# Kernel optimization log

Hardware: AMD Instinct MI355X
Metric: run time of the kernel (lower is better)

## Reference

```python
import jax, jax.numpy as jnp
import numpy as np

B, S, D_H, D_L, K, K_H, W = 4, 4096, 1024, 256, 64, 4, 9


def setup_inputs() -> dict:
    key = jax.random.key(0)
    ks = jax.random.split(key, 6)
    return {
        "inputs": jax.random.normal(ks[0], (B, S, D_H), jnp.float32),
        "W1": jax.random.normal(ks[1], (D_H, D_L), jnp.float32) * 0.02,
        "b1": jnp.zeros((D_L,), jnp.float32),
        "RME": jax.random.normal(ks[2], (D_L, K), jnp.float32),
        "K2": jax.random.normal(ks[3], (K_H, D_L, D_L), jnp.float32) * 0.02,
        "b2": jnp.zeros((D_L,), jnp.float32),
        "Wu": jax.random.normal(ks[4], (D_L, D_H), jnp.float32) * 0.02,
        "bu": jnp.zeros((D_H,), jnp.float32),
        "gamma": jnp.ones((D_H,), jnp.float32),
        "beta": jnp.zeros((D_H,), jnp.float32),
    }


def _memory_reorg(act, RMVs, k_h):
    # act: [B,S,d_l], RMVs: [B,S,k]
    R = jnp.transpose(RMVs, (0, 2, 1))  # [B,k,S]
    h_vars = jnp.mean((R - jnp.mean(R, axis=-1, keepdims=True)) ** 2, axis=-1)  # [B,k]
    top = jnp.argsort(-h_vars, axis=-1)[:, :k_h]                   # [B,k_h]
    h_max = jnp.take_along_axis(R, top[:, :, None], axis=1)        # [B,k_h,S]
    perm = jnp.argsort(h_max, axis=-1)                             # [B,k_h,S] permutation indices
    g = jnp.take_along_axis(act[:, None], perm[..., None], axis=2) # [B,k_h,S,d_l]
    return jnp.transpose(g, (0, 2, 1, 3))                          # [B,S,k_h,d_l]


def reference(inputs, W1, b1, RME, K2, b2, Wu, bu, gamma, beta):
    # DOWN_PROJECTION_1
    q = jax.nn.relu(jnp.einsum('bsh,hd->bsd', inputs, W1) + b1)    # [B,S,d_l]
    # RANDOM_PROJECTION
    RMVs = jnp.einsum('bsd,dk->bsk', q, RME)                       # [B,S,k]
    # Memory reorganization (variance-based argsort permutations)
    qp = _memory_reorg(q, RMVs, K_H)                               # [B,S,k_h,d_l]
    # DOWN_PROJECTION_2
    q2 = jax.nn.relu(jnp.einsum('bskd,kde->bse', qp, K2) + b2)     # [B,S,d_l]
    # Sliding-window key construction (edge windows replicated)
    half = (W - 1) // 2
    widx = jnp.arange(S - W + 1)[:, None] + jnp.arange(W)[None, :]  # [S-W+1, W]
    win = q2[:, widx]                                               # [B,S-W+1,W,d_l]
    first = jnp.broadcast_to(q2[:, None, :W], (B, half, W, D_L))
    last = jnp.broadcast_to(q2[:, None, S - W:], (B, half, W, D_L))
    keyt = jnp.concatenate([first, win, last], axis=1)              # [B,S,W,d_l]
    # Windowed attention
    f = jnp.sqrt(jnp.float32(D_L))
    scores = jax.nn.softmax(jnp.einsum('bsd,bswd->bsw', q2, keyt) / f, axis=-1)  # [B,S,W]
    # UP_PROJECTION on keys -> values
    val = jax.nn.relu(jnp.einsum('bswd,dh->bswh', keyt, Wu) + bu)   # [B,S,W,d_h]
    out = jnp.einsum('bswh,bsw->bsh', val, scores)                  # [B,S,d_h]
    # LayerNorm (keras default epsilon=1e-3) on residual
    x = out + inputs
    mu = jnp.mean(x, axis=-1, keepdims=True)
    var = jnp.mean((x - mu) ** 2, axis=-1, keepdims=True)
    return gamma * (x - mu) * jax.lax.rsqrt(var + 1e-3) + beta
```

## Files before the change

### kernel.cpp

```cpp
#include <hip/hip_runtime.h>

#define B_  4
#define S_  4096
#define DH  1024
#define DL  256
#define KK  64
#define KH  4
#define WW  9

typedef unsigned short ushort_t;
typedef _Float16 f16;
typedef _Float16 f16x8 __attribute__((ext_vector_type(8)));
typedef float  f32x4  __attribute__((ext_vector_type(4)));

__device__ __forceinline__ void gld_lds16(const void* g, void* lds_uniform_base) {
    __builtin_amdgcn_global_load_lds(
        (const __attribute__((address_space(1))) unsigned int*)g,
        (__attribute__((address_space(3))) unsigned int*)lds_uniform_base,
        16, 0, 0);
}

__global__ __launch_bounds__(256)
void mfma_gemm2(const float* __restrict__ Af,
                const ushort_t* __restrict__ Bh, const ushort_t* __restrict__ Bl,
                const float* __restrict__ bias, float* __restrict__ C,
                ushort_t* __restrict__ Ch, int K, int N, int nbx)
{
    __shared__ __align__(16) ushort_t Abuf[64 * 64 * 2];
    __shared__ __align__(16) ushort_t Bsh[128 * 64];
    __shared__ __align__(16) ushort_t Bsl[128 * 64];

    const int tid = threadIdx.x;
    const int w = tid >> 6, l = tid & 63;
    const int wm = w >> 1, wn = w & 1;
    const int lr = l & 15, lk = l >> 4;
    const int cpx = gridDim.x >> 3;
    const int orig = (blockIdx.x & 7) * cpx + (blockIdx.x >> 3);
    const int m0 = (orig / nbx) * 64, n0 = (orig % nbx) * 128;

    f32x4 acc0[2][4] = {};
    f32x4 acc1[2][4] = {};

    for (int k0 = 0; k0 < K; k0 += 64) {
        {
            float* Asf = (float*)Abuf;
            #pragma unroll
            for (int it = 0; it < 4; ++it) {
                const int c = it * 256 + tid;
                const int r = c >> 4, cc = c & 15;
                const int hsw = ((r & 7) << 1) | ((r >> 3) & 1);
                const int cs = cc ^ hsw;
                const float* src = Af + (size_t)(m0 + r) * K + k0 + cs * 4;
                gld_lds16(src, &Asf[(size_t)c * 4]);
            }
        }
        #pragma unroll
        for (int it = 0; it < 4; ++it) {
            const int c = it * 256 + tid;
            const int r = c >> 3, kp = c & 7;
            const int kl = kp ^ (r & 7);
            const size_t off = (size_t)(n0 + r) * K + k0 + kl * 8;
            gld_lds16(Bh + off, &Bsh[(size_t)c * 8]);
            gld_lds16(Bl + off, &Bsl[(size_t)c * 8]);
        }
        __syncthreads();

        #pragma unroll
        for (int ks = 0; ks < 2; ++ks) {
            f16x8 ah[2], al[2];
            #pragma unroll
            for (int mf = 0; mf < 2; ++mf) {
                const int row = wm * 32 + mf * 16 + lr;
                const int kb  = ks * 4 + lk;
                const float* Asf = (const float*)Abuf;
                const int base = row * 64 + ((kb ^ (row & 7)) << 3);
                const int sw = ((row >> 3) & 1) << 2;
                const f32x4 lo = *(const f32x4*)&Asf[base + sw];
                const f32x4 hi = *(const f32x4*)&Asf[base + (4 - sw)];
                const float xs[8] = {lo[0], lo[1], lo[2], lo[3],
                                     hi[0], hi[1], hi[2], hi[3]};
                #pragma unroll
                for (int e = 0; e < 8; ++e) {
                    const f16 h = (f16)xs[e];
                    const f16 lv = (f16)((xs[e] - (float)h) * 2048.0f);
                    ah[mf][e] = h;
                    al[mf][e] = lv;
                }
            }
            #pragma unroll
            for (int nf = 0; nf < 4; ++nf) {
                const int row = wn * 64 + nf * 16 + lr;
                const int kb  = ks * 4 + lk;
                const int o   = row * 64 + ((kb ^ (row & 7)) << 3);
                const f16x8 bh = *(const f16x8*)&Bsh[o];
                const f16x8 bl = *(const f16x8*)&Bsl[o];
                #pragma unroll
                for (int mf = 0; mf < 2; ++mf) {
                    acc0[mf][nf] = __builtin_amdgcn_mfma_f32_16x16x32_f16(
                        ah[mf], bh, acc0[mf][nf], 0, 0, 0);
                    acc1[mf][nf] = __builtin_amdgcn_mfma_f32_16x16x32_f16(
                        ah[mf], bl, acc1[mf][nf], 0, 0, 0);
                    acc1[mf][nf] = __builtin_amdgcn_mfma_f32_16x16x32_f16(
                        al[mf], bh, acc1[mf][nf], 0, 0, 0);
                }
            }
        }
        __syncthreads();
    }

    float bv[4];
    #pragma unroll
    for (int nf = 0; nf < 4; ++nf)
        bv[nf] = bias[n0 + wn * 64 + nf * 16 + lr];
    #pragma unroll
    for (int mf = 0; mf < 2; ++mf)
        #pragma unroll
        for (int nf = 0; nf < 4; ++nf)
            #pragma unroll
            for (int r = 0; r < 4; ++r) {
                const int m = m0 + wm * 32 + mf * 16 + lk * 4 + r;
                const int n = n0 + wn * 64 + nf * 16 + lr;
                float x = acc0[mf][nf][r] + acc1[mf][nf][r] * (1.0f / 2048.0f) + bv[nf];
                x = fmaxf(x, 0.f);
                C[(size_t)m * N + n] = x;
                const f16 h = (f16)x;
                Ch[(size_t)m * N + n] = __builtin_bit_cast(ushort_t, h);
            }
}

__global__ __launch_bounds__(256)
void gemm6_1l(const ushort_t* __restrict__ Ah, const ushort_t* __restrict__ Bh,
              const float* __restrict__ bias, ushort_t* __restrict__ Ch,
              const int* __restrict__ gidx, int K, int N, int nbx)
{
    __shared__ __align__(16) ushort_t Ash[64 * 64];
    __shared__ __align__(16) ushort_t Bsh[128 * 64];

    const int tid = threadIdx.x;
    const int w = tid >> 6, l = tid & 63;
    const int wm = w >> 1, wn = w & 1;
    const int lr = l & 15, lk = l >> 4;
    const int cpx = gridDim.x >> 3;
    const int orig = (blockIdx.x & 7) * cpx + (blockIdx.x >> 3);
    const int m0 = (orig / nbx) * 64, n0 = (orig % nbx) * 128;

    f32x4 acc0[2][4] = {};

    for (int k0 = 0; k0 < K; k0 += 64) {
        #pragma unroll
        for (int it = 0; it < 2; ++it) {
            const int c = it * 256 + tid;
            const int r = c >> 3, kp = c & 7;
            const int kl = kp ^ (r & 7);
            const int rg = gidx[(m0 + r) * KH + (k0 >> 8)];
            const size_t off = (size_t)rg * DL + (k0 & (DL - 1)) + kl * 8;
            gld_lds16(Ah + off, &Ash[(size_t)c * 8]);
        }
        #pragma unroll
        for (int it = 0; it < 4; ++it) {
            const int c = it * 256 + tid;
            const int r = c >> 3, kp = c & 7;
            const int kl = kp ^ (r & 7);
            const size_t off = (size_t)(n0 + r) * K + k0 + kl * 8;
            gld_lds16(Bh + off, &Bsh[(size_t)c * 8]);
        }
        __syncthreads();

        #pragma unroll
        for (int ks = 0; ks < 2; ++ks) {
            f16x8 ah[2];
            #pragma unroll
            for (int mf = 0; mf < 2; ++mf) {
                const int row = wm * 32 + mf * 16 + lr;
                const int kb  = ks * 4 + lk;
                ah[mf] = *(const f16x8*)&Ash[row * 64 + ((kb ^ (row & 7)) << 3)];
            }
            #pragma unroll
            for (int nf = 0; nf < 4; ++nf) {
                const int row = wn * 64 + nf * 16 + lr;
                const int kb  = ks * 4 + lk;
                const f16x8 bh = *(const f16x8*)&Bsh[row * 64 + ((kb ^ (row & 7)) << 3)];
                #pragma unroll
                for (int mf = 0; mf < 2; ++mf)
                    acc0[mf][nf] = __builtin_amdgcn_mfma_f32_16x16x32_f16(
                        ah[mf], bh, acc0[mf][nf], 0, 0, 0);
            }
        }
        __syncthreads();
    }

    float bv[4];
    #pragma unroll
    for (int nf = 0; nf < 4; ++nf)
        bv[nf] = bias[n0 + wn * 64 + nf * 16 + lr];
    #pragma unroll
    for (int mf = 0; mf < 2; ++mf)
        #pragma unroll
        for (int nf = 0; nf < 4; ++nf)
            #pragma unroll
            for (int r = 0; r < 4; ++r) {
                const int m = m0 + wm * 32 + mf * 16 + lk * 4 + r;
                const int n = n0 + wn * 64 + nf * 16 + lr;
                float x = acc0[mf][nf][r] + bv[nf];
                x = fmaxf(x, 0.f);
                const f16 h = (f16)x;
                Ch[(size_t)m * N + n] = __builtin_bit_cast(ushort_t, h);
            }
}

__global__ __launch_bounds__(512)
void mfma_gemm1l(const ushort_t* __restrict__ Ah, const ushort_t* __restrict__ Bh,
                 const float* __restrict__ bias, ushort_t* __restrict__ Ch,
                 int K, int N, int nbx)
{
    __shared__ __align__(16) ushort_t Ash[128 * 64];
    __shared__ __align__(16) ushort_t Bsh[128 * 64];

    const int tid = threadIdx.x;
    const int w = tid >> 6, l = tid & 63;
    const int wm = w >> 1, wn = w & 1;
    const int lr = l & 15, lk = l >> 4;
    const int cpx = gridDim.x >> 3;
    const int orig = (blockIdx.x & 7) * cpx + (blockIdx.x >> 3);
    const int m0 = (orig / nbx) * 128, n0 = (orig % nbx) * 128;

    f32x4 acc0[2][4] = {};

    for (int k0 = 0; k0 < K; k0 += 64) {
        #pragma unroll
        for (int it = 0; it < 2; ++it) {
            const int c = it * 512 + tid;
            const int r = c >> 3, kp = c & 7;
            const int kl = kp ^ (r & 7);
            const size_t offA = (size_t)(m0 + r) * K + k0 + kl * 8;
            const size_t offB = (size_t)(n0 + r) * K + k0 + kl * 8;
            gld_lds16(Ah + offA, &Ash[(size_t)c * 8]);
            gld_lds16(Bh + offB, &Bsh[(size_t)c * 8]);
        }
        __syncthreads();

        #pragma unroll
        for (int ks = 0; ks < 2; ++ks) {
            f16x8 ah[2];
            #pragma unroll
            for (int mf = 0; mf < 2; ++mf) {
                const int row = wm * 32 + mf * 16 + lr;
                const int kb  = ks * 4 + lk;
                ah[mf] = *(const f16x8*)&Ash[row * 64 + ((kb ^ (row & 7)) << 3)];
            }
            #pragma unroll
            for (int nf = 0; nf < 4; ++nf) {
                const int row = wn * 64 + nf * 16 + lr;
                const int kb  = ks * 4 + lk;
                const f16x8 bh = *(const f16x8*)&Bsh[row * 64 + ((kb ^ (row & 7)) << 3)];
                #pragma unroll
                for (int mf = 0; mf < 2; ++mf)
                    acc0[mf][nf] = __builtin_amdgcn_mfma_f32_16x16x32_f16(
                        ah[mf], bh, acc0[mf][nf], 0, 0, 0);
            }
        }
        __syncthreads();
    }

    float bv[4];
    #pragma unroll
    for (int nf = 0; nf < 4; ++nf)
        bv[nf] = bias[n0 + wn * 64 + nf * 16 + lr];
    #pragma unroll
    for (int mf = 0; mf < 2; ++mf)
        #pragma unroll
        for (int nf = 0; nf < 4; ++nf)
            #pragma unroll
            for (int r = 0; r < 4; ++r) {
                const int m = m0 + wm * 32 + mf * 16 + lk * 4 + r;
                const int n = n0 + wn * 64 + nf * 16 + lr;
                float x = acc0[mf][nf][r] + bv[nf];
                x = fmaxf(x, 0.f);
                const f16 hcv = (f16)x;
                Ch[(size_t)m * N + n] = __builtin_bit_cast(ushort_t, hcv);
            }
}

__global__ __launch_bounds__(256)
void tsplit2_kernel(const float* __restrict__ in, ushort_t* __restrict__ t0,
                    ushort_t* __restrict__ t1, int K, int N)
{
    __shared__ float tile[32][33];
    const int t = threadIdx.x;
    const int bk = blockIdx.x * 32, bn = blockIdx.y * 32;
    const int c = t & 31, rb = t >> 5;
    #pragma unroll
    for (int i = 0; i < 4; ++i) {
        const int r = rb + i * 8;
        tile[r][c] = in[(size_t)(bk + r) * N + bn + c];
    }
    __syncthreads();
    #pragma unroll
    for (int i = 0; i < 4; ++i) {
        const int rr = rb + i * 8;
        const float x = tile[c][rr];
        const f16 hv = (f16)x;
        const f16 lv = (f16)((x - (float)hv) * 2048.0f);
        const size_t o = (size_t)(bn + rr) * K + bk + c;
        t0[o] = __builtin_bit_cast(ushort_t, hv);
        t1[o] = __builtin_bit_cast(ushort_t, lv);
    }
}

__global__ __launch_bounds__(256)
void tsplit1_kernel(const float* __restrict__ in, ushort_t* __restrict__ t0,
                    int K, int N)
{
    __shared__ float tile[32][33];
    const int t = threadIdx.x;
    const int bk = blockIdx.x * 32, bn = blockIdx.y * 32;
    const int c = t & 31, rb = t >> 5;
    #pragma unroll
    for (int i = 0; i < 4; ++i) {
        const int r = rb + i * 8;
        tile[r][c] = in[(size_t)(bk + r) * N + bn + c];
    }
    __syncthreads();
    #pragma unroll
    for (int i = 0; i < 4; ++i) {
        const int rr = rb + i * 8;
        const f16 hv = (f16)tile[c][rr];
        t0[(size_t)(bn + rr) * K + bk + c] = __builtin_bit_cast(ushort_t, hv);
    }
}

__global__ __launch_bounds__(256)
void gemm_trans_kernel(const float* __restrict__ A, const float* __restrict__ Bm,
                       float* __restrict__ C, int M, int KA, int N)
{
    constexpr int BK = 16;
    __shared__ float Asb[BK][64 + 4];
    __shared__ float Bsb[BK][64 + 4];
    __shared__ float tileT[64][65];
    const int tid = threadIdx.x;
    const int tx = tid & 15, ty = tid >> 4;
    const int m0 = blockIdx.y * 64, n0 = blockIdx.x * 64;

    float acc[4][4] = {};
    const int lr = tid >> 2, lc = (tid & 3) << 2;
    const int kr = tid >> 4, nc = (tid & 15) << 2;

    for (int k0 = 0; k0 < KA; k0 += BK) {
        const float4 a4 = *reinterpret_cast<const float4*>(A + (size_t)(m0 + lr) * KA + k0 + lc);
        const float4 b4 = *reinterpret_cast<const float4*>(Bm + (size_t)(k0 + kr) * N + n0 + nc);
        Asb[lc + 0][lr] = a4.x; Asb[lc + 1][lr] = a4.y;
        Asb[lc + 2][lr] = a4.z; Asb[lc + 3][lr] = a4.w;
        *reinterpret_cast<float4*>(&Bsb[kr][nc]) = b4;
        __syncthreads();
        #pragma unroll
        for (int kk = 0; kk < BK; ++kk) {
            const float4 av = *reinterpret_cast<const float4*>(&Asb[kk][ty << 2]);
            const float4 bv = *reinterpret_cast<const float4*>(&Bsb[kk][tx << 2]);
            const float a[4] = {av.x, av.y, av.z, av.w};
            const float b[4] = {bv.x, bv.y, bv.z, bv.w};
            #pragma unroll
            for (int i = 0; i < 4; ++i)
                #pragma unroll
                for (int j = 0; j < 4; ++j)
                    acc[i][j] = fmaf(a[i], b[j], acc[i][j]);
        }
        __syncthreads();
    }

    #pragma unroll
    for (int i = 0; i < 4; ++i)
        #pragma unroll
        for (int j = 0; j < 4; ++j)
            tileT[(tx << 2) + j][(ty << 2) + i] = acc[i][j];
    __syncthreads();

    const int b = m0 >> 12;
    const int s0 = m0 & (S_ - 1);
    #pragma unroll
    for (int rr = 0; rr < 16; ++rr) {
        const int idx = rr * 256 + tid;
        const int kl = idx >> 6, sl = idx & 63;
        C[(size_t)(b * N + n0 + kl) * S_ + s0 + sl] = tileT[kl][sl];
    }
}

__global__ __launch_bounds__(256)
void var_kernel(const float* __restrict__ rmvT, float* __restrict__ hvars)
{
    const int bk = blockIdx.x;
    const float* src = rmvT + (size_t)bk * S_;
    float s1 = 0.f, s2 = 0.f;
    for (int t = threadIdx.x; t < S_; t += 256) {
        const float v = src[t];
        s1 += v; s2 += v * v;
    }
    #pragma unroll
    for (int off = 32; off; off >>= 1) {
        s1 += __shfl_xor(s1, off);
        s2 += __shfl_xor(s2, off);
    }
    __shared__ float r1[4], r2[4];
    const int wave = threadIdx.x >> 6, lane = threadIdx.x & 63;
    if (lane == 0) { r1[wave] = s1; r2[wave] = s2; }
    __syncthreads();
    if (threadIdx.x == 0) {
        const float t1 = r1[0] + r1[1] + r1[2] + r1[3];
        const float t2 = r2[0] + r2[1] + r2[2] + r2[3];
        const float mu = t1 / (float)S_;
        hvars[bk] = t2 / (float)S_ - mu * mu;
    }
}

__global__ void topk_kernel(const float* __restrict__ hvars, int* __restrict__ topidx)
{
    const int b = threadIdx.x;
    if (b >= B_) return;
    float v[KK];
    for (int k = 0; k < KK; ++k) v[k] = hvars[b * KK + k];
    for (int i = 0; i < KH; ++i) {
        int best = 0; float bv = -3.4e38f;
        for (int k = 0; k < KK; ++k)
            if (v[k] > bv) { bv = v[k]; best = k; }
        topidx[b * KH + i] = best;
        v[best] = -3.4e38f;
    }
}

__global__ __launch_bounds__(256)
void rank_kernel(const float* __restrict__ rmvT, const int* __restrict__ topidx,
                 int* __restrict__ gidx)
{
    const int bi = blockIdx.x;
    const int b = bi >> 2, ih = bi & 3;
    const int k = topidx[b * KH + ih];
    const float* src = rmvT + (size_t)(b * KK + k) * S_;
    __shared__ __align__(16) unsigned long long keys[S_];
    __shared__ int partial[4][64];
    for (int t = threadIdx.x; t < S_; t += 256) {
        const unsigned bits = __builtin_bit_cast(unsigned, src[t]);
        const unsigned u = (bits & 0x80000000u) ? ~bits : (bits | 0x80000000u);
        keys[t] = ((unsigned long long)u << 12) | (unsigned)t;
    }
    __syncthreads();

    const int il = threadIdx.x & 63;
    const int chunk = threadIdx.x >> 6;
    const int i = blockIdx.y * 64 + il;
    const unsigned long long ki = keys[i];

    int cnt = 0;
    const int jbase = chunk << 10;
    #pragma unroll 8
    for (int jj = 0; jj < 1024; jj += 2) {
        const ulonglong2 k2 = *reinterpret_cast<const ulonglong2*>(&keys[jbase + jj]);
        cnt += (int)(k2.x < ki);
        cnt += (int)(k2.y < ki);
    }
    partial[chunk][il] = cnt;
    __syncthreads();
    if (threadIdx.x < 64) {
        const int rank = partial[0][threadIdx.x] + partial[1][threadIdx.x]
                       + partial[2][threadIdx.x] + partial[3][threadIdx.x];
        const int ii = blockIdx.y * 64 + threadIdx.x;
        gidx[((b << 12) + rank) * KH + ih] = (b << 12) + ii;
    }
}

__global__ __launch_bounds__(256)
void final_kernel(const ushort_t* __restrict__ vh, const ushort_t* __restrict__ q2h,
                  const float* __restrict__ inputs, const float* __restrict__ gamma,
                  const float* __restrict__ beta, float* __restrict__ out)
{
    const int bid = blockIdx.x;
    const int m0 = (((bid & 7) << 9) | (bid >> 3)) << 2;
    const int wave = threadIdx.x >> 6, lane = threadIdx.x & 63;
    const int m = m0 + wave;
    const int s = m & (S_ - 1), b = m >> 12;
    const int jb = (s < 4) ? 0 : (s >= S_ - 4 ? S_ - WW : s - 4);

    const ushort_t* vb = vh + (size_t)(b * S_ + jb) * DH;
    const float* inp = inputs + (size_t)m * DH;
    f16x8 varr[2][WW];
    float4 iv[2][2];
    #pragma unroll
    for (int c = 0; c < 2; ++c) {
        const int h = (c << 9) + (lane << 3);
        #pragma unroll
        for (int w = 0; w < WW; ++w)
            varr[c][w] = *reinterpret_cast<const f16x8*>(vb + (size_t)w * DH + h);
        iv[c][0] = *reinterpret_cast<const float4*>(inp + h);
        iv[c][1] = *reinterpret_cast<const float4*>(inp + h + 4);
    }

    const ushort4 qv4 = *reinterpret_cast<const ushort4*>(q2h + (size_t)m * DL + (lane << 2));
    const float qx = (float)__builtin_bit_cast(f16, qv4.x);
    const float qy = (float)__builtin_bit_cast(f16, qv4.y);
    const float qz = (float)__builtin_bit_cast(f16, qv4.z);
    const float qw = (float)__builtin_bit_cast(f16, qv4.w);
    const ushort_t* kbase = q2h + (size_t)(b * S_ + jb) * DL;
    float sc[WW];
    #pragma unroll
    for (int w = 0; w < WW; ++w) {
        const ushort4 kv4 = *reinterpret_cast<const ushort4*>(kbase + w * DL + (lane << 2));
        float d = qx * (float)__builtin_bit_cast(f16, kv4.x)
                + qy * (float)__builtin_bit_cast(f16, kv4.y)
                + qz * (float)__builtin_bit_cast(f16, kv4.z)
                + qw * (float)__builtin_bit_cast(f16, kv4.w);
        #pragma unroll
        for (int off = 32; off; off >>= 1) d += __shfl_xor(d, off);
        sc[w] = d * 0.0625f;
    }
    float mx = sc[0];
    #pragma unroll
    for (int w = 1; w < WW; ++w) mx = fmaxf(mx, sc[w]);
    float wgt[WW]; float sum = 0.f;
    #pragma unroll
    for (int w = 0; w < WW; ++w) { wgt[w] = __expf(sc[w] - mx); sum += wgt[w]; }
    const float inv = 1.f / sum;
    #pragma unroll
    for (int w = 0; w < WW; ++w) wgt[w] *= inv;

    float x[2][8];
    float s1 = 0.f, s2 = 0.f;
    #pragma unroll
    for (int c = 0; c < 2; ++c) {
        float acc[8] = {};
        #pragma unroll
        for (int w = 0; w < WW; ++w) {
            const f16x8 vv = varr[c][w];
            #pragma unroll
            for (int e = 0; e < 8; ++e)
                acc[e] = fmaf(wgt[w], (float)vv[e], acc[e]);
        }
        #pragma unroll
        for (int e = 0; e < 8; ++e) {
            const float ivv = (e < 4) ? (&iv[c][0].x)[e] : (&iv[c][1].x)[e - 4];
            acc[e] += ivv;
            x[c][e] = acc[e];
            s1 += acc[e];
            s2 += acc[e] * acc[e];
        }
    }

    #pragma unroll
    for (int off = 32; off; off >>= 1) {
        s1 += __shfl_xor(s1, off);
        s2 += __shfl_xor(s2, off);
    }
    const float mu = s1 / (float)DH;
    const float rs = rsqrtf(s2 / (float)DH - mu * mu + 0.001f);

    #pragma unroll
    for (int c = 0; c < 2; ++c) {
        const int h = (c << 9) + (lane << 3);
        #pragma unroll
        for (int half = 0; half < 2; ++half) {
            const float4 g  = *reinterpret_cast<const float4*>(gamma + h + half * 4);
            const float4 bt = *reinterpret_cast<const float4*>(beta + h + half * 4);
            float4 o;
            o.x = g.x * (x[c][half * 4 + 0] - mu) * rs + bt.x;
            o.y = g.y * (x[c][half * 4 + 1] - mu) * rs + bt.y;
            o.z = g.z * (x[c][half * 4 + 2] - mu) * rs + bt.z;
            o.w = g.w * (x[c][half * 4 + 3] - mu) * rs + bt.w;
            *reinterpret_cast<float4*>(out + (size_t)m * DH + h + half * 4) = o;
        }
    }
}

extern "C" void kernel_launch(void* const* d_in, const int* in_sizes, int n_in,
                              void* d_out, int out_size, void* d_ws, size_t ws_size,
                              hipStream_t stream)
{
    (void)in_sizes; (void)n_in; (void)out_size; (void)ws_size;
    const float* inputs = (const float*)d_in[0];
    const float* W1     = (const float*)d_in[1];
    const float* b1     = (const float*)d_in[2];
    const float* RME    = (const float*)d_in[3];
    const float* K2     = (const float*)d_in[4];
    const float* b2     = (const float*)d_in[5];
    const float* Wu     = (const float*)d_in[6];
    const float* bu     = (const float*)d_in[7];
    const float* gamma  = (const float*)d_in[8];
    const float* beta   = (const float*)d_in[9];
    float* out = (float*)d_out;

    char* ws = (char*)d_ws;
    const size_t MB = 1u << 20;
    ushort_t* vh  = (ushort_t*)(ws + 0 * MB);
    float*    q   = (float*)   (ws + 64 * MB);
    ushort_t* qh  = (ushort_t*)(ws + 80 * MB);
    ushort_t* q2h = (ushort_t*)(ws + 112 * MB);
    float*    rmvT= (float*)   (ws + 128 * MB);
    float*    hvars  = (float*)(ws + 132 * MB);
    int*      topidx = (int*)  (ws + 132 * MB + 4096);
    int*      gidx   = (int*)  (ws + 132 * MB + 8192);
    ushort_t* w1th = (ushort_t*)(ws + 133 * MB);
    ushort_t* w1tl = w1th + (DH * DL);
    ushort_t* k2th = w1tl + (DH * DL);
    ushort_t* wuth = k2th + (KH * DL * DL);

    const int M = B_ * S_;

    tsplit2_kernel<<<dim3(DH / 32, DL / 32), dim3(256), 0, stream>>>(W1, w1th, w1tl, DH, DL);
    tsplit1_kernel<<<dim3(KH * DL / 32, DL / 32), dim3(256), 0, stream>>>((const float*)K2, k2th, KH * DL, DL);
    tsplit1_kernel<<<dim3(DL / 32, DH / 32), dim3(256), 0, stream>>>(Wu, wuth, DL, DH);

    mfma_gemm2<<<dim3((DL / 128) * (M / 64)), dim3(256), 0, stream>>>(
        inputs, w1th, w1tl, b1, q, qh, DH, DL, DL / 128);
    gemm_trans_kernel<<<dim3(KK / 64, M / 64), dim3(256), 0, stream>>>(q, RME, rmvT, M, DL, KK);
    var_kernel<<<dim3(B_ * KK), dim3(256), 0, stream>>>(rmvT, hvars);
    topk_kernel<<<dim3(1), dim3(64), 0, stream>>>(hvars, topidx);
    rank_kernel<<<dim3(B_ * KH, S_ / 64), dim3(256), 0, stream>>>(rmvT, topidx, gidx);
    gemm6_1l<<<dim3((DL / 128) * (M / 64)), dim3(256), 0, stream>>>(
        qh, k2th, b2, q2h, gidx, KH * DL, DL, DL / 128);
    mfma_gemm1l<<<dim3((DH / 128) * (M / 128)), dim3(512), 0, stream>>>(
        q2h, wuth, bu, vh, DL, DH, DH / 128);
    final_kernel<<<dim3(M / 4), dim3(256), 0, stream>>>(vh, q2h, inputs, gamma, beta, out);
}
```

Measured before the change: 166.5 us.

## Split-K the first down-projection GEMM and process two rows per wave in final kernel

The first GEMM (inputs x W1) is split along K into two halves with twice as many blocks. Each half writes a partial fp32 plane, and a new reduce kernel adds the planes, applies bias and ReLU, and emits fp32 and fp16 copies of q. This aims to fill more CUs, since the original grid had only 512 blocks, at the cost of extra partial-sum traffic and one more launch. Separately, the final attention/LayerNorm kernel now has each wave handle two adjacent rows, sharing the 10 overlapping window loads of keys and values to cut redundant global reads.

New measurement: 180.0 us. +8.1%, slower.

```diff
diff --git a/kernel.cpp b/kernel.cpp
--- a/kernel.cpp
+++ b/kernel.cpp
@@ -21,10 +21,9 @@
 }
 
 __global__ __launch_bounds__(256)
-void mfma_gemm2(const float* __restrict__ Af,
-                const ushort_t* __restrict__ Bh, const ushort_t* __restrict__ Bl,
-                const float* __restrict__ bias, float* __restrict__ C,
-                ushort_t* __restrict__ Ch, int K, int N, int nbx)
+void mfma_gemm2sk(const float* __restrict__ Af,
+                  const ushort_t* __restrict__ Bh, const ushort_t* __restrict__ Bl,
+                  float* __restrict__ Cp, int K, int N, int nbx)
 {
     __shared__ __align__(16) ushort_t Abuf[64 * 64 * 2];
     __shared__ __align__(16) ushort_t Bsh[128 * 64];
@@ -36,12 +35,15 @@
     const int lr = l & 15, lk = l >> 4;
     const int cpx = gridDim.x >> 3;
     const int orig = (blockIdx.x & 7) * cpx + (blockIdx.x >> 3);
-    const int m0 = (orig / nbx) * 64, n0 = (orig % nbx) * 128;
+    const int kb = orig & 1;
+    const int o2 = orig >> 1;
+    const int m0 = (o2 / nbx) * 64, n0 = (o2 % nbx) * 128;
+    const int kbase = kb * (K >> 1);
 
     f32x4 acc0[2][4] = {};
     f32x4 acc1[2][4] = {};
 
-    for (int k0 = 0; k0 < K; k0 += 64) {
+    for (int k0 = 0; k0 < (K >> 1); k0 += 64) {
         {
             float* Asf = (float*)Abuf;
             #pragma unroll
@@ -50,7 +52,7 @@
                 const int r = c >> 4, cc = c & 15;
                 const int hsw = ((r & 7) << 1) | ((r >> 3) & 1);
                 const int cs = cc ^ hsw;
-                const float* src = Af + (size_t)(m0 + r) * K + k0 + cs * 4;
+                const float* src = Af + (size_t)(m0 + r) * K + kbase + k0 + cs * 4;
                 gld_lds16(src, &Asf[(size_t)c * 4]);
             }
         }
@@ -59,7 +61,7 @@
             const int c = it * 256 + tid;
             const int r = c >> 3, kp = c & 7;
             const int kl = kp ^ (r & 7);
-            const size_t off = (size_t)(n0 + r) * K + k0 + kl * 8;
+            const size_t off = (size_t)(n0 + r) * K + kbase + k0 + kl * 8;
             gld_lds16(Bh + off, &Bsh[(size_t)c * 8]);
             gld_lds16(Bl + off, &Bsl[(size_t)c * 8]);
         }
@@ -71,9 +73,9 @@
             #pragma unroll
             for (int mf = 0; mf < 2; ++mf) {
                 const int row = wm * 32 + mf * 16 + lr;
-                const int kb  = ks * 4 + lk;
+                const int kb2 = ks * 4 + lk;
                 const float* Asf = (const float*)Abuf;
-                const int base = row * 64 + ((kb ^ (row & 7)) << 3);
+                const int base = row * 64 + ((kb2 ^ (row & 7)) << 3);
                 const int sw = ((row >> 3) & 1) << 2;
                 const f32x4 lo = *(const f32x4*)&Asf[base + sw];
                 const f32x4 hi = *(const f32x4*)&Asf[base + (4 - sw)];
@@ -90,8 +92,8 @@
             #pragma unroll
             for (int nf = 0; nf < 4; ++nf) {
                 const int row = wn * 64 + nf * 16 + lr;
-                const int kb  = ks * 4 + lk;
-                const int o   = row * 64 + ((kb ^ (row & 7)) << 3);
+                const int kb2 = ks * 4 + lk;
+                const int o   = row * 64 + ((kb2 ^ (row & 7)) << 3);
                 const f16x8 bh = *(const f16x8*)&Bsh[o];
                 const f16x8 bl = *(const f16x8*)&Bsl[o];
                 #pragma unroll
@@ -108,10 +110,7 @@
         __syncthreads();
     }
 
-    float bv[4];
-    #pragma unroll
-    for (int nf = 0; nf < 4; ++nf)
-        bv[nf] = bias[n0 + wn * 64 + nf * 16 + lr];
+    float* plane = Cp + (size_t)kb * ((size_t)B_ * S_ * DL);
     #pragma unroll
     for (int mf = 0; mf < 2; ++mf)
         #pragma unroll
@@ -120,12 +119,31 @@
             for (int r = 0; r < 4; ++r) {
                 const int m = m0 + wm * 32 + mf * 16 + lk * 4 + r;
                 const int n = n0 + wn * 64 + nf * 16 + lr;
-                float x = acc0[mf][nf][r] + acc1[mf][nf][r] * (1.0f / 2048.0f) + bv[nf];
-                x = fmaxf(x, 0.f);
-                C[(size_t)m * N + n] = x;
-                const f16 h = (f16)x;
-                Ch[(size_t)m * N + n] = __builtin_bit_cast(ushort_t, h);
-            }
+                plane[(size_t)m * N + n] = acc0[mf][nf][r] + acc1[mf][nf][r] * (1.0f / 2048.0f);
+            }
+}
+
+__global__ __launch_bounds__(256)
+void reduce_q(const float* __restrict__ p, const float* __restrict__ bias,
+              float* __restrict__ q, ushort_t* __restrict__ qh)
+{
+    const int i = blockIdx.x * 256 + threadIdx.x;
+    const float4 p0 = ((const float4*)p)[i];
+    const float4 p1 = ((const float4*)p)[i + 1048576];
+    const int n0 = (i << 2) & (DL - 1);
+    const float4 bv = *reinterpret_cast<const float4*>(bias + n0);
+    float4 x;
+    x.x = fmaxf(p0.x + p1.x + bv.x, 0.f);
+    x.y = fmaxf(p0.y + p1.y + bv.y, 0.f);
+    x.z = fmaxf(p0.z + p1.z + bv.z, 0.f);
+    x.w = fmaxf(p0.w + p1.w + bv.w, 0.f);
+    ((float4*)q)[i] = x;
+    ushort4 h;
+    h.x = __builtin_bit_cast(ushort_t, (f16)x.x);
+    h.y = __builtin_bit_cast(ushort_t, (f16)x.y);
+    h.z = __builtin_bit_cast(ushort_t, (f16)x.z);
+    h.w = __builtin_bit_cast(ushort_t, (f16)x.w);
+    *(ushort4*)&qh[(size_t)i * 4] = h;
 }
 
 __global__ __launch_bounds__(256)
@@ -472,97 +490,134 @@
                   const float* __restrict__ beta, float* __restrict__ out)
 {
     const int bid = blockIdx.x;
-    const int m0 = (((bid & 7) << 9) | (bid >> 3)) << 2;
+    const int mb = (((bid & 7) << 8) | (bid >> 3)) << 3;
     const int wave = threadIdx.x >> 6, lane = threadIdx.x & 63;
-    const int m = m0 + wave;
-    const int s = m & (S_ - 1), b = m >> 12;
-    const int jb = (s < 4) ? 0 : (s >= S_ - 4 ? S_ - WW : s - 4);
-
-    const ushort_t* vb = vh + (size_t)(b * S_ + jb) * DH;
-    const float* inp = inputs + (size_t)m * DH;
-    f16x8 varr[2][WW];
-    float4 iv[2][2];
+    const int m = mb + wave * 2;
+    const int s0 = m & (S_ - 1), b = m >> 12;
+    const int s1r = s0 + 1;
+    const int jb0 = (s0  < 4) ? 0 : (s0  >= S_ - 4 ? S_ - WW : s0  - 4);
+    const int jb1 = (s1r < 4) ? 0 : (s1r >= S_ - 4 ? S_ - WW : s1r - 4);
+    const int off1 = jb1 - jb0;
+
+    ushort4 qwin[10];
+    #pragma unroll
+    for (int k = 0; k < 10; ++k) {
+        int jr = jb0 + k; if (jr > S_ - 1) jr = S_ - 1;
+        qwin[k] = *reinterpret_cast<const ushort4*>(q2h + (size_t)(b * S_ + jr) * DL + (lane << 2));
+    }
+    float wgt[2][WW];
+    #pragma unroll
+    for (int r = 0; r < 2; ++r) {
+        const ushort4 qv4 = *reinterpret_cast<const ushort4*>(q2h + (size_t)(m + r) * DL + (lane << 2));
+        const float qx = (float)__builtin_bit_cast(f16, qv4.x);
+        const float qy = (float)__builtin_bit_cast(f16, qv4.y);
+        const float qz = (float)__builtin_bit_cast(f16, qv4.z);
+        const float qw = (float)__builtin_bit_cast(f16, qv4.w);
+        float sc[WW];
+        if (r == 1 && off1 == 1) {
+            #pragma unroll
+            for (int w = 0; w < WW; ++w) {
+                const ushort4 kv4 = qwin[w + 1];
+                float d = qx * (float)__builtin_bit_cast(f16, kv4.x)
+                        + qy * (float)__builtin_bit_cast(f16, kv4.y)
+                        + qz * (float)__builtin_bit_cast(f16, kv4.z)
+                        + qw * (float)__builtin_bit_cast(f16, kv4.w);
+                #pragma unroll
+                for (int off = 32; off; off >>= 1) d += __shfl_xor(d, off);
+                sc[w] = d * 0.0625f;
+            }
+        } else {
+            #pragma unroll
+            for (int w = 0; w < WW; ++w) {
+                const ushort4 kv4 = qwin[w];
+                float d = qx * (float)__builtin_bit_cast(f16, kv4.x)
+                        + qy * (float)__builtin_bit_cast(f16, kv4.y)
+                        + qz * (float)__builtin_bit_cast(f16, kv4.z)
+                        + qw * (float)__builtin_bit_cast(f16, kv4.w);
+                #pragma unroll
+                for (int off = 32; off; off >>= 1) d += __shfl_xor(d, off);
+                sc[w] = d * 0.0625f;
+            }
+        }
+        float mx = sc[0];
+        #pragma unroll
+        for (int w = 1; w < WW; ++w) mx = fmaxf(mx, sc[w]);
+        float sum = 0.f;
+        #pragma unroll
+        for (int w = 0; w < WW; ++w) { wgt[r][w] = __expf(sc[w] - mx); sum += wgt[r][w]; }
+        const float inv = 1.f / sum;
+        #pragma unroll
+        for (int w = 0; w < WW; ++w) wgt[r][w] *= inv;
+    }
+
+    float x[2][2][8];
+    float s1acc[2] = {0.f, 0.f}, s2acc[2] = {0.f, 0.f};
     #pragma unroll
     for (int c = 0; c < 2; ++c) {
         const int h = (c << 9) + (lane << 3);
-        #pragma unroll
-        for (int w = 0; w < WW; ++w)
-            varr[c][w] = *reinterpret_cast<const f16x8*>(vb + (size_t)w * DH + h);
-        iv[c][0] = *reinterpret_cast<const float4*>(inp + h);
-        iv[c][1] = *reinterpret_cast<const float4*>(inp + h + 4);
-    }
-
-    const ushort4 qv4 = *reinterpret_cast<const ushort4*>(q2h + (size_t)m * DL + (lane << 2));
-    const float qx = (float)__builtin_bit_cast(f16, qv4.x);
-    const float qy = (float)__builtin_bit_cast(f16, qv4.y);
-    const float qz = (float)__builtin_bit_cast(f16, qv4.z);
-    const float qw = (float)__builtin_bit_cast(f16, qv4.w);
-    const ushort_t* kbase = q2h + (size_t)(b * S_ + jb) * DL;
-    float sc[WW];
-    #pragma unroll
-    for (int w = 0; w < WW; ++w) {
-        const ushort4 kv4 = *reinterpret_cast<const ushort4*>(kbase + w * DL + (lane << 2));
-        float d = qx * (float)__builtin_bit_cast(f16, kv4.x)
-                + qy * (float)__builtin_bit_cast(f16, kv4.y)
-                + qz * (float)__builtin_bit_cast(f16, kv4.z)
-                + qw * (float)__builtin_bit_cast(f16, kv4.w);
-        #pragma unroll
-        for (int off = 32; off; off >>= 1) d += __shfl_xor(d, off);
-        sc[w] = d * 0.0625f;
-    }
-    float mx = sc[0];
-    #pragma unroll
-    for (int w = 1; w < WW; ++w) mx = fmaxf(mx, sc[w]);
-    float wgt[WW]; float sum = 0.f;
-    #pragma unroll
-    for (int w = 0; w < WW; ++w) { wgt[w] = __expf(sc[w] - mx); sum += wgt[w]; }
-    const float inv = 1.f / sum;
-    #pragma unroll
-    for (int w = 0; w < WW; ++w) wgt[w] *= inv;
-
-    float x[2][8];
-    float s1 = 0.f, s2 = 0.f;
-    #pragma unroll
-    for (int c = 0; c < 2; ++c) {
-        float acc[8] = {};
-        #pragma unroll
-        for (int w = 0; w < WW; ++w) {
-            const f16x8 vv = varr[c][w];
-            #pragma unroll
-            for (int e = 0; e < 8; ++e)
-                acc[e] = fmaf(wgt[w], (float)vv[e], acc[e]);
-        }
-        #pragma unroll
-        for (int e = 0; e < 8; ++e) {
-            const float ivv = (e < 4) ? (&iv[c][0].x)[e] : (&iv[c][1].x)[e - 4];
-            acc[e] += ivv;
-            x[c][e] = acc[e];
-            s1 += acc[e];
-            s2 += acc[e] * acc[e];
-        }
-    }
-
-    #pragma unroll
-    for (int off = 32; off; off >>= 1) {
-        s1 += __shfl_xor(s1, off);
-        s2 += __shfl_xor(s2, off);
-    }
-    const float mu = s1 / (float)DH;
-    const float rs = rsqrtf(s2 / (float)DH - mu * mu + 0.001f);
-
-    #pragma unroll
-    for (int c = 0; c < 2; ++c) {
-        const int h = (c << 9) + (lane << 3);
-        #pragma unroll
-        for (int half = 0; half < 2; ++half) {
-            const float4 g  = *reinterpret_cast<const float4*>(gamma + h + half * 4);
-            const float4 bt = *reinterpret_cast<const float4*>(beta + h + half * 4);
-            float4 o;
-            o.x = g.x * (x[c][half * 4 + 0] - mu) * rs + bt.x;
-            o.y = g.y * (x[c][half * 4 + 1] - mu) * rs + bt.y;
-            o.z = g.z * (x[c][half * 4 + 2] - mu) * rs + bt.z;
-            o.w = g.w * (x[c][half * 4 + 3] - mu) * rs + bt.w;
-            *reinterpret_cast<float4*>(out + (size_t)m * DH + h + half * 4) = o;
+        f16x8 va[10];
+        #pragma unroll
+        for (int k = 0; k < 10; ++k) {
+            int jr = jb0 + k; if (jr > S_ - 1) jr = S_ - 1;
+            va[k] = *reinterpret_cast<const f16x8*>(vh + (size_t)(b * S_ + jr) * DH + h);
+        }
+        #pragma unroll
+        for (int r = 0; r < 2; ++r) {
+            float acc[8] = {};
+            if (r == 1 && off1 == 1) {
+                #pragma unroll
+                for (int w = 0; w < WW; ++w) {
+                    const f16x8 vv = va[w + 1];
+                    #pragma unroll
+                    for (int e = 0; e < 8; ++e)
+                        acc[e] = fmaf(wgt[r][w], (float)vv[e], acc[e]);
+                }
+            } else {
+                #pragma unroll
+                for (int w = 0; w < WW; ++w) {
+                    const f16x8 vv = va[w];
+                    #pragma unroll
+                    for (int e = 0; e < 8; ++e)
+                        acc[e] = fmaf(wgt[r][w], (float)vv[e], acc[e]);
+                }
+            }
+            const float4 iv0 = *reinterpret_cast<const float4*>(inputs + (size_t)(m + r) * DH + h);
+            const float4 iv1 = *reinterpret_cast<const float4*>(inputs + (size_t)(m + r) * DH + h + 4);
+            #pragma unroll
+            for (int e = 0; e < 8; ++e) {
+                const float ivv = (e < 4) ? (&iv0.x)[e] : (&iv1.x)[e - 4];
+                acc[e] += ivv;
+                x[r][c][e] = acc[e];
+                s1acc[r] += acc[e];
+                s2acc[r] += acc[e] * acc[e];
+            }
+        }
+    }
+
+    #pragma unroll
+    for (int r = 0; r < 2; ++r) {
+        float s1 = s1acc[r], s2 = s2acc[r];
+        #pragma unroll
+        for (int off = 32; off; off >>= 1) {
+            s1 += __shfl_xor(s1, off);
+            s2 += __shfl_xor(s2, off);
+        }
+        const float mu = s1 / (float)DH;
+        const float rs = rsqrtf(s2 / (float)DH - mu * mu + 0.001f);
+        #pragma unroll
+        for (int c = 0; c < 2; ++c) {
+            const int h = (c << 9) + (lane << 3);
+            #pragma unroll
+            for (int half = 0; half < 2; ++half) {
+                const float4 g  = *reinterpret_cast<const float4*>(gamma + h + half * 4);
+                const float4 bt = *reinterpret_cast<const float4*>(beta + h + half * 4);
+                float4 o;
+                o.x = g.x * (x[r][c][half * 4 + 0] - mu) * rs + bt.x;
+                o.y = g.y * (x[r][c][half * 4 + 1] - mu) * rs + bt.y;
+                o.z = g.z * (x[r][c][half * 4 + 2] - mu) * rs + bt.z;
+                o.w = g.w * (x[r][c][half * 4 + 3] - mu) * rs + bt.w;
+                *reinterpret_cast<float4*>(out + (size_t)(m + r) * DH + h + half * 4) = o;
+            }
         }
     }
 }
@@ -586,11 +641,12 @@
 
     char* ws = (char*)d_ws;
     const size_t MB = 1u << 20;
-    ushort_t* vh  = (ushort_t*)(ws + 0 * MB);
-    float*    q   = (float*)   (ws + 64 * MB);
-    ushort_t* qh  = (ushort_t*)(ws + 80 * MB);
-    ushort_t* q2h = (ushort_t*)(ws + 112 * MB);
-    float*    rmvT= (float*)   (ws + 128 * MB);
+    ushort_t* vh    = (ushort_t*)(ws + 0 * MB);
+    float*    qpart = (float*)   (ws + 32 * MB);
+    float*    q     = (float*)   (ws + 64 * MB);
+    ushort_t* qh    = (ushort_t*)(ws + 80 * MB);
+    ushort_t* q2h   = (ushort_t*)(ws + 112 * MB);
+    float*    rmvT  = (float*)   (ws + 128 * MB);
     float*    hvars  = (float*)(ws + 132 * MB);
     int*      topidx = (int*)  (ws + 132 * MB + 4096);
     int*      gidx   = (int*)  (ws + 132 * MB + 8192);
@@ -605,8 +661,9 @@
     tsplit1_kernel<<<dim3(KH * DL / 32, DL / 32), dim3(256), 0, stream>>>((const float*)K2, k2th, KH * DL, DL);
     tsplit1_kernel<<<dim3(DL / 32, DH / 32), dim3(256), 0, stream>>>(Wu, wuth, DL, DH);
 
-    mfma_gemm2<<<dim3((DL / 128) * (M / 64)), dim3(256), 0, stream>>>(
-        inputs, w1th, w1tl, b1, q, qh, DH, DL, DL / 128);
+    mfma_gemm2sk<<<dim3((DL / 128) * (M / 64) * 2), dim3(256), 0, stream>>>(
+        inputs, w1th, w1tl, qpart, DH, DL, DL / 128);
+    reduce_q<<<dim3(M * DL / 1024), dim3(256), 0, stream>>>(qpart, b1, q, qh);
     gemm_trans_kernel<<<dim3(KK / 64, M / 64), dim3(256), 0, stream>>>(q, RME, rmvT, M, DL, KK);
     var_kernel<<<dim3(B_ * KK), dim3(256), 0, stream>>>(rmvT, hvars);
     topk_kernel<<<dim3(1), dim3(64), 0, stream>>>(hvars, topidx);
@@ -615,5 +672,5 @@
         qh, k2th, b2, q2h, gidx, KH * DL, DL, DL / 128);
     mfma_gemm1l<<<dim3((DH / 128) * (M / 128)), dim3(512), 0, stream>>>(
         q2h, wuth, bu, vh, DL, DH, DH / 128);
-    final_kernel<<<dim3(M / 4), dim3(256), 0, stream>>>(vh, q2h, inputs, gamma, beta, out);
-}
+    final_kernel<<<dim3(M / 8), dim3(256), 0, stream>>>(vh, q2h, inputs, gamma, beta, out);
+}
```
